# Kernel optimization log

Measured on AMD Instinct MI355X. Metric: run time of the kernel, lower is better.

The kernel has to match this reference:

```python
import jax, jax.numpy as jnp
import numpy as np

B, D, Q, E, H, V = 32, 1024, 64, 384, 384, 50000
PAD = 0
EPS = 1e-12


def setup_inputs() -> dict:
    key = jax.random.key(0)
    ks = jax.random.split(key, 13)
    documents = jax.random.randint(ks[0], (B, D), 1, V)
    doc_lens = jax.random.randint(ks[1], (B,), D // 2, D + 1)
    doc_valid = jnp.arange(D)[None, :] < doc_lens[:, None]
    documents = jnp.where(doc_valid, documents, PAD)
    doc_masks = doc_valid.astype(jnp.float32)[:, :, None]
    querys = jax.random.randint(ks[2], (B, Q), 1, V)
    query_lens = jax.random.randint(ks[3], (B,), Q // 2, Q + 1)
    q_valid = jnp.arange(Q)[None, :] < query_lens[:, None]
    querys = jnp.where(q_valid, querys, PAD)
    query_masks = q_valid.astype(jnp.float32)[:, :, None]
    answers = documents[:, :1]  # guaranteed present in each doc
    emb = jax.random.uniform(ks[4], (V + 1, E), jnp.float32, -0.05, 0.05)
    emb = emb.at[PAD].set(0.0)
    gw = lambda k, s: jax.random.normal(k, s, jnp.float32) * 0.05
    w_ih_f = gw(ks[5], (3 * H, E)); w_hh_f = gw(ks[6], (3 * H, H))
    b_ih_f = gw(ks[7], (3 * H,)); b_hh_f = gw(ks[8], (3 * H,))
    w_ih_b = gw(ks[9], (3 * H, E)); w_hh_b = gw(ks[10], (3 * H, H))
    b_ih_b = gw(ks[11], (3 * H,)); b_hh_b = gw(ks[12], (3 * H,))
    return dict(documents=documents, doc_lens=doc_lens, doc_masks=doc_masks,
                querys=querys, query_lens=query_lens, query_masks=query_masks,
                answers=answers, emb=emb,
                w_ih_f=w_ih_f, w_hh_f=w_hh_f, b_ih_f=b_ih_f, b_hh_f=b_hh_f,
                w_ih_b=w_ih_b, w_hh_b=w_hh_b, b_ih_b=b_ih_b, b_hh_b=b_hh_b)


def _gru_dir(x, w_ih, w_hh, b_ih, b_hh):
    # x: [B,T,E] -> outputs [B,T,H]; torch GRU cell math
    Bn = x.shape[0]
    Hn = w_hh.shape[1]
    xp = jnp.einsum('bte,ge->btg', x, w_ih) + b_ih  # precompute input projections [B,T,3H]

    def step(h, g):
        gh = h @ w_hh.T + b_hh
        i_r, i_z, i_n = jnp.split(g, 3, axis=-1)
        h_r, h_z, h_n = jnp.split(gh, 3, axis=-1)
        r = jax.nn.sigmoid(i_r + h_r)
        z = jax.nn.sigmoid(i_z + h_z)
        n = jnp.tanh(i_n + r * h_n)
        hn = (1.0 - z) * n + z * h
        return hn, hn

    h0 = jnp.zeros((Bn, Hn), x.dtype)
    _, out = jax.lax.scan(step, h0, jnp.swapaxes(xp, 0, 1))
    return jnp.swapaxes(out, 0, 1)


def _rev_within_len(x, lens):
    # reverse each sequence only over its valid prefix (emulates packed bwd GRU)
    T = x.shape[1]
    t = jnp.arange(T)
    idx = jnp.where(t[None, :] < lens[:, None], lens[:, None] - 1 - t[None, :], t[None, :])
    return jnp.take_along_axis(x, idx[:, :, None], axis=1)


def _bigru(x, lens, valid, pf, pb):
    out_f = _gru_dir(x, *pf)
    out_b = _rev_within_len(_gru_dir(_rev_within_len(x, lens), *pb), lens)
    out = jnp.concatenate([out_f, out_b], axis=-1)
    return out * valid[:, :, None]  # unpack pads with zeros


def _softmax_mask(x, mask, axis):
    shift = jnp.max(x, axis=axis, keepdims=True)
    e = jnp.exp(x - shift) * mask
    return e / (jnp.sum(e, axis=axis, keepdims=True) + EPS)


def reference(documents, doc_lens, doc_masks, querys, query_lens, query_masks, answers,
              emb, w_ih_f, w_hh_f, b_ih_f, b_hh_f, w_ih_b, w_hh_b, b_ih_b, b_hh_b):
    doc_valid = doc_masks[..., 0]
    q_valid = query_masks[..., 0]
    doc_h = _bigru(emb[documents], doc_lens, doc_valid,
                   (w_ih_f, w_hh_f, b_ih_f, b_hh_f), (w_ih_b, w_hh_b, b_ih_b, b_hh_b))
    q_h = _bigru(emb[querys], query_lens, q_valid,
                 (w_ih_f, w_hh_f, b_ih_f, b_hh_f), (w_ih_b, w_hh_b, b_ih_b, b_hh_b))
    scores = jnp.einsum('bdh,bqh->bdq', doc_h, q_h)          # IndiATT_output
    pair_mask = jnp.einsum('bdo,bqo->bdq', doc_masks, query_masks)
    alpha = _softmax_mask(scores, pair_mask, axis=1)
    beta = _softmax_mask(scores, pair_mask, axis=2)
    beta_aver = jnp.sum(beta, axis=1) / doc_lens[:, None].astype(scores.dtype)  # [B,Q]
    s = jnp.einsum('bdq,bq->bd', alpha, beta_aver)            # AoA_output squeezed
    probs = jnp.sum(s * (documents == answers).astype(s.dtype), axis=1)

    def pick(doc, sv, vv):
        sc = jnp.zeros(V + 1, s.dtype).at[doc].add(sv * vv)   # segment-sum by word id
        cnt = jnp.zeros(V + 1, s.dtype).at[doc].add(vv)
        return jnp.argmax(jnp.where(cnt > 0, sc, -jnp.inf))

    pred_answers = jax.vmap(pick)(documents, s, doc_valid)
    return probs, pred_answers
```

## Files before the change

kernel.cpp:

```cpp
#include <hip/hip_runtime.h>
#include <hip/hip_bf16.h>
#include <stdint.h>

#define EPSV 1e-12f
#define NB 32
#define DD 1024
#define QQ 64
#define EE 384
#define HH 384
#define NW 12
#define CH 256
#define XPBUF ((size_t)2 * CH * 36864)

typedef __attribute__((ext_vector_type(4))) float f32x4;
typedef __attribute__((ext_vector_type(8))) __bf16 bf16x8;
typedef __attribute__((ext_vector_type(4))) unsigned short u16x4;
typedef __attribute__((ext_vector_type(4))) int i32x4;
typedef unsigned short u16;

static __device__ __forceinline__ u16 f2bf(float f) {
  union { float f; uint32_t u; } v; v.f = f;
  uint32_t u = v.u;
  return (u16)((u + 0x7fffu + ((u >> 16) & 1u)) >> 16);
}

static __device__ __forceinline__ f32x4 MFMA(bf16x8 a, bf16x8 b, f32x4 c) {
  return __builtin_amdgcn_mfma_f32_16x16x32_bf16(a, b, c, 0, 0, 0);
}

static __device__ __forceinline__ bf16x8 ldw8(const float* p) {
  float4 a = *(const float4*)p;
  float4 b = *(const float4*)(p + 4);
  union { u16 e[8]; bf16x8 v; } u;
  u.e[0] = f2bf(a.x); u.e[1] = f2bf(a.y); u.e[2] = f2bf(a.z); u.e[3] = f2bf(a.w);
  u.e[4] = f2bf(b.x); u.e[5] = f2bf(b.y); u.e[6] = f2bf(b.z); u.e[7] = f2bf(b.w);
  return u.v;
}

static __device__ __forceinline__ void st_short_sc(u16* p, u16 v) {
  asm volatile("global_store_short %0, %1, off sc1" :: "v"(p), "v"((uint32_t)v) : "memory");
}
static __device__ __forceinline__ void ld_b128_sc(const u16* p, i32x4& d) {
  asm volatile("global_load_dwordx4 %0, %1, off sc1" : "=v"(d) : "v"(p) : "memory");
}
static __device__ __forceinline__ void st_dword_sc(unsigned* p, unsigned v) {
  asm volatile("global_store_dword %0, %1, off sc1" :: "v"(p), "v"(v) : "memory");
}
static __device__ __forceinline__ void ld_tags(const unsigned* p, i32x4& a, i32x4& b, i32x4& c,
                                               i32x4& d, i32x4& e, i32x4& f) {
  asm volatile(
      "global_load_dwordx4 %0, %6, off sc1\n\t"
      "global_load_dwordx4 %1, %6, off offset:16 sc1\n\t"
      "global_load_dwordx4 %2, %6, off offset:32 sc1\n\t"
      "global_load_dwordx4 %3, %6, off offset:48 sc1\n\t"
      "global_load_dwordx4 %4, %6, off offset:64 sc1\n\t"
      "global_load_dwordx4 %5, %6, off offset:80 sc1\n\t"
      "s_waitcnt vmcnt(0)"
      : "=&v"(a), "=&v"(b), "=&v"(c), "=&v"(d), "=&v"(e), "=&v"(f)
      : "v"(p) : "memory");
}

__global__ __launch_bounds__(256) void k_emb(const int* __restrict__ doc, const int* __restrict__ qry,
                                             const float* __restrict__ emb, u16* __restrict__ embx) {
  int i = blockIdx.x * 256 + threadIdx.x;
  int row = i / 96, e4 = i - row * 96;
  int tok = (row < NB * DD) ? doc[row] : qry[row - NB * DD];
  float4 v = ((const float4*)(emb + (size_t)tok * EE))[e4];
  u16x4 o; o.x = f2bf(v.x); o.y = f2bf(v.y); o.z = f2bf(v.z); o.w = f2bf(v.w);
  *(u16x4*)(embx + (size_t)row * EE + e4 * 4) = o;
}

__global__ __launch_bounds__(512, 2) void k_xp(
    const u16* __restrict__ embx, const int* __restrict__ doc_lens, const int* __restrict__ q_lens,
    const float* __restrict__ w_ih_f, const float* __restrict__ b_ih_f, const float* __restrict__ b_hh_f,
    const float* __restrict__ w_ih_b, const float* __restrict__ b_ih_b, const float* __restrict__ b_hh_b,
    float* __restrict__ xpd, float* __restrict__ xpq, int cbase) {
  __shared__ int lensh[32];
  const int gx = blockIdx.x;
  int corpus, d2, jblk, tch;
  if (gx < 48) { corpus = 0; d2 = gx / 24; int rem = gx % 24; jblk = rem / 4; tch = rem % 4; }
  else { corpus = 1; int g2 = gx - 48; d2 = g2 / 6; jblk = g2 % 6; tch = 0; }
  const int T = corpus ? QQ : DD;
  const int* lens = corpus ? q_lens : doc_lens;
  const float* w_ih = d2 ? w_ih_b : w_ih_f;
  const float* b_ih = d2 ? b_ih_b : b_ih_f;
  const float* b_hh = d2 ? b_hh_b : b_hh_f;
  const u16* exb = embx + (corpus ? (size_t)NB * DD * EE : 0);
  float* xpg = corpus ? (xpq + (size_t)d2 * QQ * 36864) : (xpd + (size_t)d2 * CH * 36864);
  const int tid = threadIdx.x;
  if (tid < 32) lensh[tid] = lens[tid];
  __syncthreads();
  const int lane = tid & 63, wv = tid >> 6;
  const int wslot = wv >> 1, mt = wv & 1;
  const int col = lane & 15, khi = lane >> 4;
  const int jg = jblk * 64 + wslot * 16 + col;
  const float br = b_ih[jg] + b_hh[jg];
  const float bz = b_ih[384 + jg] + b_hh[384 + jg];
  const float bn = b_ih[768 + jg];
  bf16x8 Wr[12], Wz[12], Wn[12];
#pragma unroll
  for (int ks = 0; ks < 12; ++ks) {
    Wr[ks] = ldw8(w_ih + (size_t)jg * 384 + ks * 32 + khi * 8);
    Wz[ks] = ldw8(w_ih + (size_t)(384 + jg) * 384 + ks * 32 + khi * 8);
    Wn[ks] = ldw8(w_ih + (size_t)(768 + jg) * 384 + ks * 32 + khi * 8);
  }
  const int b_a = mt * 16 + col;
  const int lenb = lensh[b_a];
  const int bh0 = mt * 16 + khi * 4;
  for (int tt = 0; tt < 64; ++tt) {
    const int s_lc = tch * 64 + tt;
    const int s_g = corpus ? s_lc : (cbase + s_lc);
    const int trow = d2 ? ((s_g < lenb) ? (lenb - 1 - s_g) : s_g) : s_g;
    const u16* ap = exb + ((size_t)b_a * T + trow) * EE + khi * 8;
    bf16x8 A[12];
#pragma unroll
    for (int ks = 0; ks < 12; ++ks) A[ks] = *(const bf16x8*)(ap + ks * 32);
    f32x4 ar{0.f, 0.f, 0.f, 0.f}, az = ar, an = ar;
#pragma unroll
    for (int ks = 0; ks < 12; ++ks) {
      ar = MFMA(A[ks], Wr[ks], ar);
      az = MFMA(A[ks], Wz[ks], az);
      an = MFMA(A[ks], Wn[ks], an);
    }
    float* op = xpg + (size_t)s_lc * 36864 + (size_t)jg * 32 + bh0;
    f32x4 o0{ar[0] + br, ar[1] + br, ar[2] + br, ar[3] + br};
    f32x4 o1{az[0] + bz, az[1] + bz, az[2] + bz, az[3] + bz};
    f32x4 o2{an[0] + bn, an[1] + bn, an[2] + bn, an[3] + bn};
    *(f32x4*)op = o0;
    *(f32x4*)(op + 384 * 32) = o1;
    *(f32x4*)(op + 768 * 32) = o2;
  }
}

__global__ __launch_bounds__(256) void k_rec(
    const float* __restrict__ xp_rd, float* __restrict__ xp_wr, const float* __restrict__ xpq,
    const int* __restrict__ doc_lens, const int* __restrict__ q_lens,
    const float* __restrict__ w_hh_f, const float* __restrict__ b_hh_f,
    const float* __restrict__ w_hh_b, const float* __restrict__ b_hh_b,
    u16* __restrict__ doc_h, u16* __restrict__ q_h,
    u16* __restrict__ h_bc, unsigned* __restrict__ cnts, unsigned* __restrict__ tags,
    float* __restrict__ h_state,
    const u16* __restrict__ embx,
    const float* __restrict__ w_ih_f, const float* __restrict__ b_ih_f,
    const float* __restrict__ w_ih_b, const float* __restrict__ b_ih_b,
    int cbase, int first, int rec_blocks) {
  __shared__ u16 wfrag[36864];
  __shared__ int lensh[32];
  const int bid = blockIdx.x;
  const int tid = threadIdx.x;

  if (bid >= rec_blocks) {
    const int e = bid - rec_blocks;
    const int d2 = e / 48;
    const int rem = e - d2 * 48;
    const int jb = rem >> 2, tch = rem & 3;
    const float* w_ih = d2 ? w_ih_b : w_ih_f;
    const float* b_ih = d2 ? b_ih_b : b_ih_f;
    const float* b_hh2 = d2 ? b_hh_b : b_hh_f;
    float* xpo = xp_wr + (size_t)d2 * CH * 36864;
    if (tid < 32) lensh[tid] = doc_lens[tid];
    __syncthreads();
    const int lane = tid & 63, wv = tid >> 6;
    const int wslot = wv >> 1, mt = wv & 1;
    const int col = lane & 15, khi = lane >> 4;
    const int jg = jb * 32 + wslot * 16 + col;
    const float br = b_ih[jg] + b_hh2[jg];
    const float bz = b_ih[384 + jg] + b_hh2[384 + jg];
    const float bn = b_ih[768 + jg];
    bf16x8 Wr[12], Wz[12], Wn[12];
#pragma unroll
    for (int ks = 0; ks < 12; ++ks) {
      Wr[ks] = ldw8(w_ih + (size_t)jg * 384 + ks * 32 + khi * 8);
      Wz[ks] = ldw8(w_ih + (size_t)(384 + jg) * 384 + ks * 32 + khi * 8);
      Wn[ks] = ldw8(w_ih + (size_t)(768 + jg) * 384 + ks * 32 + khi * 8);
    }
    const int b_a = mt * 16 + col;
    const int lenb = lensh[b_a];
    const int bh0 = mt * 16 + khi * 4;
    const int cb2 = cbase + CH;
    for (int tt = 0; tt < 64; ++tt) {
      const int s_lc = tch * 64 + tt;
      const int s_g = cb2 + s_lc;
      const int trow = d2 ? ((s_g < lenb) ? (lenb - 1 - s_g) : s_g) : s_g;
      const u16* ap = embx + ((size_t)b_a * DD + trow) * EE + khi * 8;
      bf16x8 A[12];
#pragma unroll
      for (int ks = 0; ks < 12; ++ks) A[ks] = *(const bf16x8*)(ap + ks * 32);
      f32x4 ar{0.f, 0.f, 0.f, 0.f}, az = ar, an = ar;
#pragma unroll
      for (int ks = 0; ks < 12; ++ks) {
        ar = MFMA(A[ks], Wr[ks], ar);
        az = MFMA(A[ks], Wz[ks], az);
        an = MFMA(A[ks], Wn[ks], an);
      }
      float* op = xpo + (size_t)s_lc * 36864 + (size_t)jg * 32 + bh0;
      f32x4 o0{ar[0] + br, ar[1] + br, ar[2] + br, ar[3] + br};
      f32x4 o1{az[0] + bz, az[1] + bz, az[2] + bz, az[3] + bz};
      f32x4 o2{an[0] + bn, an[1] + bn, an[2] + bn, an[3] + bn};
      *(f32x4*)op = o0;
      *(f32x4*)(op + 384 * 32) = o1;
      *(f32x4*)(op + 768 * 32) = o2;
    }
    return;
  }

  const int grp = bid / NW;
  const int wg = bid - grp * NW;
  const int corpus = grp >> 1, dir = grp & 1;
  const int T = corpus ? QQ : DD;
  const int nst = corpus ? QQ : CH;
  const int* lens = corpus ? q_lens : doc_lens;
  const float* w_hh = dir ? w_hh_b : w_hh_f;
  const float* b_hh = dir ? b_hh_b : b_hh_f;
  u16* out = corpus ? q_h : doc_h;
  const float* xpg = corpus ? (xpq + (size_t)dir * QQ * 36864) : (xp_rd + (size_t)dir * CH * 36864);
  u16* hb = h_bc + (size_t)grp * (2 * NB * HH);
  unsigned* cnt = cnts + (size_t)grp * 16;

  if (tid < 32) lensh[tid] = lens[tid];
  for (int idx = tid; idx < 36864; idx += 256) {
    int nt = idx / 6144;
    int rem = idx - nt * 6144;
    int ks = rem >> 9;
    int le = rem & 511;
    int lane_ = le >> 3, i = le & 7;
    int g = nt >> 1, js_ = nt & 1;
    int colw = lane_ & 15;
    int k = ks * 32 + (lane_ >> 4) * 8 + i;
    int rowg = g * 384 + wg * 32 + js_ * 16 + colw;
    wfrag[idx] = f2bf(w_hh[(size_t)rowg * 384 + k]);
  }
  if (first) {
    for (int idx = tid; idx < 1024; idx += 256) {
      int b = idx >> 5, jl_ = idx & 31;
      st_short_sc(hb + b * HH + wg * 32 + jl_, (u16)0);
    }
    asm volatile("s_waitcnt vmcnt(0)" ::: "memory");
  }
  __syncthreads();
  if (first) {
    if (tid == 0) {
      __hip_atomic_fetch_add(cnt, 1u, __ATOMIC_RELAXED, __HIP_MEMORY_SCOPE_AGENT);
      while (__hip_atomic_load(cnt, __ATOMIC_RELAXED, __HIP_MEMORY_SCOPE_AGENT) < (unsigned)NW)
        __builtin_amdgcn_s_sleep(1);
    }
    __syncthreads();
  }

  const int lane = tid & 63, wv = tid >> 6;
  const int mt = wv >> 1, js = wv & 1;
  const int col = lane & 15, khi = lane >> 4;
  const int jg = wg * 32 + js * 16 + col;
  const float bias_hn = b_hh[768 + jg];
  const int b_x = mt * 16 + col;
  const int bh0 = mt * 16 + khi * 4;
  int len_h[4];
#pragma unroll
  for (int r = 0; r < 4; ++r) len_h[r] = lensh[bh0 + r];
  u16* outp = out + (size_t)dir * HH + jg;
  f32x4 hprev;
#pragma unroll
  for (int r = 0; r < 4; ++r)
    hprev[r] = first ? 0.f : h_state[(size_t)grp * 12288 + (size_t)jg * 32 + (bh0 + r)];

  const unsigned* tagrow = tags + (size_t)grp * 64 + mt * 32;
  unsigned* tagp = tags + (size_t)grp * 64 + mt * 32 + (wg * 2 + js);

  auto umin2 = [](unsigned a, unsigned b) { return a < b ? a : b; };
  auto pollwait = [&](unsigned need) {
    while (true) {
      i32x4 t0, t1, t2, t3, t4, t5;
      ld_tags(tagrow, t0, t1, t2, t3, t4, t5);
      unsigned mn = 0xffffffffu;
#pragma unroll
      for (int k = 0; k < 4; ++k) {
        mn = umin2(mn, (unsigned)t0[k]); mn = umin2(mn, (unsigned)t1[k]);
        mn = umin2(mn, (unsigned)t2[k]); mn = umin2(mn, (unsigned)t3[k]);
        mn = umin2(mn, (unsigned)t4[k]); mn = umin2(mn, (unsigned)t5[k]);
      }
      if (mn >= need) break;
      __builtin_amdgcn_s_sleep(1);
    }
  };
  auto load_xp = [&](f32x4* x, int sl) {
    const float* xs = xpg + (size_t)sl * 36864;
#pragma unroll
    for (int g = 0; g < 3; ++g)
      x[g] = *(const f32x4*)(xs + ((size_t)(g * 384 + jg)) * 32 + bh0);
  };

  f32x4 xpA[3], xpB[3];
  load_xp(xpA, 0);

  auto step = [&](int sl, f32x4* xc, f32x4* xn) {
    const int s = cbase + sl;
    const int p = s & 1;
    const u16* rbuf = hb + p * (NB * HH);
    u16* wbuf = hb + (p ^ 1) * (NB * HH);
    pollwait((unsigned)s);
    i32x4 areg[12];
    const u16* ahp = rbuf + b_x * HH + khi * 8;
#pragma unroll
    for (int ks = 0; ks < 12; ++ks) ld_b128_sc(ahp + ks * 32, areg[ks]);
    asm volatile("s_waitcnt vmcnt(0)" ::: "memory");
    __builtin_amdgcn_sched_barrier(0);
    f32x4 acc_r{0.f, 0.f, 0.f, 0.f};
    f32x4 acc_z = acc_r, acc_nh = acc_r;
#pragma unroll
    for (int ks = 0; ks < 12; ++ks) {
      bf16x8 af = __builtin_bit_cast(bf16x8, areg[ks]);
      bf16x8 br = *(const bf16x8*)&wfrag[((js) * 12 + ks) * 512 + lane * 8];
      bf16x8 bz = *(const bf16x8*)&wfrag[((2 + js) * 12 + ks) * 512 + lane * 8];
      bf16x8 bn = *(const bf16x8*)&wfrag[((4 + js) * 12 + ks) * 512 + lane * 8];
      acc_r = MFMA(af, br, acc_r);
      acc_z = MFMA(af, bz, acc_z);
      acc_nh = MFMA(af, bn, acc_nh);
    }
    u16 hq[4];
#pragma unroll
    for (int r = 0; r < 4; ++r) {
      const int b = bh0 + r;
      float rg = 1.f / (1.f + __expf(-(acc_r[r] + xc[0][r])));
      float zg = 1.f / (1.f + __expf(-(acc_z[r] + xc[1][r])));
      float ng = tanhf(xc[2][r] + rg * (acc_nh[r] + bias_hn));
      float hn = (1.f - zg) * ng + zg * hprev[r];
      hprev[r] = hn;
      hq[r] = f2bf(hn);
      st_short_sc(wbuf + b * HH + jg, hq[r]);
    }
    asm volatile("s_waitcnt vmcnt(0)" ::: "memory");
    if (lane == 0) st_dword_sc(tagp, (unsigned)(s + 1));
    load_xp(xn, (sl + 1 < nst) ? (sl + 1) : sl);
#pragma unroll
    for (int r = 0; r < 4; ++r) {
      const int b = bh0 + r;
      const int len = len_h[r];
      const int tro = dir ? ((s < len) ? (len - 1 - s) : s) : s;
      outp[((size_t)b * T + tro) * (2 * HH)] = hq[r];
    }
  };

  for (int sl = 0; sl < nst; sl += 2) {
    step(sl, xpA, xpB);
    step(sl + 1, xpB, xpA);
  }
#pragma unroll
  for (int r = 0; r < 4; ++r)
    h_state[(size_t)grp * 12288 + (size_t)jg * 32 + (bh0 + r)] = hprev[r];
}

__global__ __launch_bounds__(256) void k_scores(
    const u16* __restrict__ doc_h, const u16* __restrict__ q_h,
    const int* __restrict__ doc_lens, const int* __restrict__ q_lens,
    float* __restrict__ SM, float* __restrict__ rowmax, float* __restrict__ rowsum) {
  const int b = blockIdx.x >> 4, dblk = blockIdx.x & 15;
  const int tid = threadIdx.x, lane = tid & 63, wv = tid >> 6;
  const int col = lane & 15, khi = lane >> 4;
  const int dlen = doc_lens[b], qlen = q_lens[b];
  const u16* dp = doc_h + ((size_t)(b * DD + dblk * 64 + wv * 16 + col)) * (2 * HH) + khi * 8;
  const u16* qp = q_h + (size_t)b * QQ * (2 * HH);
  f32x4 acc[4];
#pragma unroll
  for (int nt = 0; nt < 4; ++nt) acc[nt] = f32x4{0.f, 0.f, 0.f, 0.f};
  for (int ks = 0; ks < 24; ++ks) {
    bf16x8 av = *(const bf16x8*)(dp + ks * 32);
#pragma unroll
    for (int nt = 0; nt < 4; ++nt) {
      bf16x8 bv = *(const bf16x8*)(qp + (size_t)(nt * 16 + col) * (2 * HH) + ks * 32 + khi * 8);
      acc[nt] = MFMA(av, bv, acc[nt]);
    }
  }
  const int d0 = dblk * 64 + wv * 16 + khi * 4;
  float* smb = SM + (size_t)b * DD * QQ;
#pragma unroll
  for (int r = 0; r < 4; ++r) {
    const int d = d0 + r;
    const bool dv = d < dlen;
    float v[4];
#pragma unroll
    for (int nt = 0; nt < 4; ++nt) {
      const int q = nt * 16 + col;
      v[nt] = (dv && q < qlen) ? acc[nt][r] : 0.f;
      smb[(size_t)d * QQ + q] = v[nt];
    }
    float mx = fmaxf(fmaxf(v[0], v[1]), fmaxf(v[2], v[3]));
#pragma unroll
    for (int off = 1; off < 16; off <<= 1) mx = fmaxf(mx, __shfl_xor(mx, off, 64));
    float sm = 0.f;
#pragma unroll
    for (int nt = 0; nt < 4; ++nt) {
      const int q = nt * 16 + col;
      if (dv && q < qlen) sm += __expf(v[nt] - mx);
    }
#pragma unroll
    for (int off = 1; off < 16; off <<= 1) sm += __shfl_xor(sm, off, 64);
    if (col == 0) { rowmax[b * DD + d] = mx; rowsum[b * DD + d] = sm; }
  }
}

__global__ __launch_bounds__(256) void k_cols(
    const float* __restrict__ SM, const float* __restrict__ rowmax, const float* __restrict__ rowsum,
    const int* __restrict__ doc_lens, const int* __restrict__ q_lens,
    float* __restrict__ colmax, float* __restrict__ colsum, float* __restrict__ bav) {
  const int b = blockIdx.x, tid = threadIdx.x;
  const int q = tid & 63, dg = tid >> 6;
  __shared__ float red[4][64];
  __shared__ float cmx[64];
  const float* smb = SM + (size_t)b * DD * QQ;
  float cm = -3.0e38f;
  for (int d = dg; d < DD; d += 4) cm = fmaxf(cm, smb[(size_t)d * QQ + q]);
  red[dg][q] = cm;
  __syncthreads();
  if (tid < 64) cmx[tid] = fmaxf(fmaxf(red[0][tid], red[1][tid]), fmaxf(red[2][tid], red[3][tid]));
  __syncthreads();
  const int dlen = doc_lens[b];
  const bool qv = q < q_lens[b];
  const float cmq = cmx[q];
  float cs = 0.f, ba = 0.f;
  for (int d = dg; d < DD; d += 4) {
    if (qv && d < dlen) {
      float v = smb[(size_t)d * QQ + q];
      cs += __expf(v - cmq);
      ba += __expf(v - rowmax[b * DD + d]) / (rowsum[b * DD + d] + EPSV);
    }
  }
  __syncthreads();
  red[dg][q] = cs;
  __syncthreads();
  float cst = 0.f;
  if (tid < 64) cst = red[0][tid] + red[1][tid] + red[2][tid] + red[3][tid];
  __syncthreads();
  red[dg][q] = ba;
  __syncthreads();
  if (tid < 64) {
    float bat = red[0][tid] + red[1][tid] + red[2][tid] + red[3][tid];
    colmax[b * QQ + tid] = cmx[tid];
    colsum[b * QQ + tid] = cst;
    bav[b * QQ + tid] = bat / (float)dlen;
  }
}

__global__ __launch_bounds__(256) void k_s(
    const float* __restrict__ SM, const float* __restrict__ colmax, const float* __restrict__ colsum,
    const float* __restrict__ bav, const int* __restrict__ doc_lens, const int* __restrict__ q_lens,
    const int* __restrict__ documents, const int* __restrict__ answers,
    float* __restrict__ sc, float* __restrict__ cnt_tok, float* __restrict__ dout) {
  const int b = blockIdx.x >> 2, dblk = blockIdx.x & 3;
  const int tid = threadIdx.x;
  __shared__ float cm[64], cs[64], bv[64];
  __shared__ int qm[64];
  if (tid < 64) {
    cm[tid] = colmax[b * QQ + tid];
    cs[tid] = colsum[b * QQ + tid];
    bv[tid] = bav[b * QQ + tid];
    qm[tid] = (tid < q_lens[b]) ? 1 : 0;
  }
  __syncthreads();
  const int d = dblk * 256 + tid;
  const bool dv = d < doc_lens[b];
  const float* smr = SM + ((size_t)b * DD + d) * QQ;
  float sd = 0.f;
#pragma unroll
  for (int q = 0; q < 64; ++q) {
    float e = (dv && qm[q]) ? __expf(smr[q] - cm[q]) : 0.f;
    sd += e / (cs[q] + EPSV) * bv[q];
  }
  const int tok = documents[b * DD + d];
  if (tok == answers[b]) atomicAdd(&dout[b], sd);
  if (dv) {
    atomicAdd(&sc[(size_t)b * 50001 + tok], sd);
    atomicAdd(&cnt_tok[(size_t)b * 50001 + tok], 1.0f);
  }
}

__global__ __launch_bounds__(256) void k_pred(
    const float* __restrict__ sc, const float* __restrict__ cnt_tok, float* __restrict__ dout) {
  const int b = blockIdx.x, tid = threadIdx.x;
  __shared__ float bvs[256];
  __shared__ int bis[256];
  float bvv = -3.0e38f;
  int bii = 0x7fffffff;
  for (int i = tid; i < 50001; i += 256) {
    if (cnt_tok[(size_t)b * 50001 + i] > 0.f) {
      float v = sc[(size_t)b * 50001 + i];
      if (v > bvv) { bvv = v; bii = i; }
    }
  }
  bvs[tid] = bvv;
  bis[tid] = bii;
  __syncthreads();
  for (int st = 128; st > 0; st >>= 1) {
    if (tid < st) {
      float v2 = bvs[tid + st];
      int i2 = bis[tid + st];
      if (v2 > bvs[tid] || (v2 == bvs[tid] && i2 < bis[tid])) { bvs[tid] = v2; bis[tid] = i2; }
    }
    __syncthreads();
  }
  if (tid == 0) dout[32 + b] = (float)bis[0];
}

extern "C" void kernel_launch(void* const* d_in, const int* in_sizes, int n_in,
                              void* d_out, int out_size, void* d_ws, size_t ws_size,
                              hipStream_t stream) {
  const int* documents = (const int*)d_in[0];
  const int* doc_lens = (const int*)d_in[1];
  const int* querys = (const int*)d_in[3];
  const int* query_lens = (const int*)d_in[4];
  const int* answers = (const int*)d_in[6];
  const float* emb = (const float*)d_in[7];
  const float* w_ih_f = (const float*)d_in[8];
  const float* w_hh_f = (const float*)d_in[9];
  const float* b_ih_f = (const float*)d_in[10];
  const float* b_hh_f = (const float*)d_in[11];
  const float* w_ih_b = (const float*)d_in[12];
  const float* w_hh_b = (const float*)d_in[13];
  const float* b_ih_b = (const float*)d_in[14];
  const float* b_hh_b = (const float*)d_in[15];
  float* dout = (float*)d_out;
  char* ws = (char*)d_ws;

  size_t o = 0;
  auto alloc = [&](size_t bytes) { size_t r = o; o += (bytes + 255) & ~(size_t)255; return r; };
  size_t o_embx = alloc((size_t)34816 * 384 * 2);
  size_t o_xpd  = alloc((size_t)2 * XPBUF * 4);
  size_t o_xpq  = alloc((size_t)2 * QQ * 36864 * 4);
  size_t o_doch = alloc((size_t)NB * DD * 768 * 2);
  size_t o_qh   = alloc((size_t)NB * QQ * 768 * 2);
  size_t o_hbc  = alloc((size_t)4 * 2 * NB * HH * 2);
  size_t o_hst  = alloc((size_t)4 * HH * NB * 4);
  size_t o_cnt  = alloc((size_t)4 * 16 * 4);
  size_t o_tag  = alloc((size_t)4 * 64 * 4);
  size_t o_sync_end = o;
  size_t o_SM   = alloc((size_t)NB * DD * QQ * 4);
  size_t o_rmax = alloc((size_t)NB * DD * 4);
  size_t o_rsum = alloc((size_t)NB * DD * 4);
  size_t o_cmax = alloc((size_t)NB * QQ * 4);
  size_t o_csum = alloc((size_t)NB * QQ * 4);
  size_t o_bav  = alloc((size_t)NB * QQ * 4);
  size_t o_sc   = alloc((size_t)NB * 50001 * 4);
  size_t o_ctk  = alloc((size_t)NB * 50001 * 4);
  (void)ws_size; (void)in_sizes; (void)n_in; (void)out_size;

  hipMemsetAsync(ws + o_cnt, 0, o_sync_end - o_cnt, stream);
  hipMemsetAsync(ws + o_sc, 0, (o_ctk - o_sc) + (size_t)NB * 50001 * 4, stream);
  hipMemsetAsync(d_out, 0, 64 * sizeof(float), stream);

  k_emb<<<13056, 256, 0, stream>>>(documents, querys, emb, (u16*)(ws + o_embx));
  k_xp<<<60, 512, 0, stream>>>((u16*)(ws + o_embx), doc_lens, query_lens,
                               w_ih_f, b_ih_f, b_hh_f, w_ih_b, b_ih_b, b_hh_b,
                               (float*)(ws + o_xpd), (float*)(ws + o_xpq), 0);
  for (int c = 0; c < 4; ++c) {
    const int rec_blocks = (c == 0) ? 48 : 24;
    const int xp_blocks = (c < 3) ? 96 : 0;
    float* xp_rd = (float*)(ws + o_xpd) + (size_t)(c & 1) * XPBUF;
    float* xp_wr = (float*)(ws + o_xpd) + (size_t)((c + 1) & 1) * XPBUF;
    k_rec<<<rec_blocks + xp_blocks, 256, 0, stream>>>(
        xp_rd, xp_wr, (float*)(ws + o_xpq), doc_lens, query_lens,
        w_hh_f, b_hh_f, w_hh_b, b_hh_b,
        (u16*)(ws + o_doch), (u16*)(ws + o_qh),
        (u16*)(ws + o_hbc), (unsigned*)(ws + o_cnt), (unsigned*)(ws + o_tag),
        (float*)(ws + o_hst),
        (u16*)(ws + o_embx), w_ih_f, b_ih_f, w_ih_b, b_ih_b,
        c * CH, c == 0 ? 1 : 0, rec_blocks);
  }
  k_scores<<<512, 256, 0, stream>>>((u16*)(ws + o_doch), (u16*)(ws + o_qh), doc_lens, query_lens,
                                    (float*)(ws + o_SM), (float*)(ws + o_rmax), (float*)(ws + o_rsum));
  k_cols<<<32, 256, 0, stream>>>((float*)(ws + o_SM), (float*)(ws + o_rmax), (float*)(ws + o_rsum),
                                 doc_lens, query_lens,
                                 (float*)(ws + o_cmax), (float*)(ws + o_csum), (float*)(ws + o_bav));
  k_s<<<128, 256, 0, stream>>>((float*)(ws + o_SM), (float*)(ws + o_cmax), (float*)(ws + o_csum),
                               (float*)(ws + o_bav), doc_lens, query_lens, documents, answers,
                               (float*)(ws + o_sc), (float*)(ws + o_ctk), dout);
  k_pred<<<32, 256, 0, stream>>>((float*)(ws + o_sc), (float*)(ws + o_ctk), dout);
}
```

Baseline: 5.285 ms.

## Halve recurrent workgroups per GRU direction, doubling hidden columns per block

Each recurrent group now uses 6 workgroups instead of 12. Each workgroup holds 64 hidden columns of W_hh in LDS (twice the previous footprint) and issues six MFMA chains per wave per step instead of three. The per-step cross-workgroup tag poll now reads 12 tags instead of 24, and the first chunk launches half as many recurrent blocks. The aim is to cut inter-block synchronisation latency on the serial time loop. The cost is more work per block on the critical path and LDS use close to the per-block limit.

```diff
diff --git a/kernel.cpp b/kernel.cpp
--- a/kernel.cpp
+++ b/kernel.cpp
@@ -8,7 +8,7 @@
 #define QQ 64
 #define EE 384
 #define HH 384
-#define NW 12
+#define NW 6
 #define CH 256
 #define XPBUF ((size_t)2 * CH * 36864)
 
@@ -46,17 +46,13 @@
 static __device__ __forceinline__ void st_dword_sc(unsigned* p, unsigned v) {
   asm volatile("global_store_dword %0, %1, off sc1" :: "v"(p), "v"(v) : "memory");
 }
-static __device__ __forceinline__ void ld_tags(const unsigned* p, i32x4& a, i32x4& b, i32x4& c,
-                                               i32x4& d, i32x4& e, i32x4& f) {
+static __device__ __forceinline__ void ld_tags3(const unsigned* p, i32x4& a, i32x4& b, i32x4& c) {
   asm volatile(
-      "global_load_dwordx4 %0, %6, off sc1\n\t"
-      "global_load_dwordx4 %1, %6, off offset:16 sc1\n\t"
-      "global_load_dwordx4 %2, %6, off offset:32 sc1\n\t"
-      "global_load_dwordx4 %3, %6, off offset:48 sc1\n\t"
-      "global_load_dwordx4 %4, %6, off offset:64 sc1\n\t"
-      "global_load_dwordx4 %5, %6, off offset:80 sc1\n\t"
+      "global_load_dwordx4 %0, %3, off sc1\n\t"
+      "global_load_dwordx4 %1, %3, off offset:16 sc1\n\t"
+      "global_load_dwordx4 %2, %3, off offset:32 sc1\n\t"
       "s_waitcnt vmcnt(0)"
-      : "=&v"(a), "=&v"(b), "=&v"(c), "=&v"(d), "=&v"(e), "=&v"(f)
+      : "=&v"(a), "=&v"(b), "=&v"(c)
       : "v"(p) : "memory");
 }
 
@@ -144,7 +140,7 @@
     const float* __restrict__ w_ih_f, const float* __restrict__ b_ih_f,
     const float* __restrict__ w_ih_b, const float* __restrict__ b_ih_b,
     int cbase, int first, int rec_blocks) {
-  __shared__ u16 wfrag[36864];
+  __shared__ u16 wfrag[73728];
   __shared__ int lensh[32];
   const int bid = blockIdx.x;
   const int tid = threadIdx.x;
@@ -218,22 +214,22 @@
   unsigned* cnt = cnts + (size_t)grp * 16;
 
   if (tid < 32) lensh[tid] = lens[tid];
-  for (int idx = tid; idx < 36864; idx += 256) {
-    int nt = idx / 6144;
-    int rem = idx - nt * 6144;
+  for (int idx = tid; idx < 73728; idx += 256) {
+    int t = idx / 6144;
+    int rem = idx - t * 6144;
     int ks = rem >> 9;
     int le = rem & 511;
     int lane_ = le >> 3, i = le & 7;
-    int g = nt >> 1, js_ = nt & 1;
+    int g = t >> 2, sl = t & 3;
     int colw = lane_ & 15;
     int k = ks * 32 + (lane_ >> 4) * 8 + i;
-    int rowg = g * 384 + wg * 32 + js_ * 16 + colw;
+    int rowg = g * 384 + wg * 64 + sl * 16 + colw;
     wfrag[idx] = f2bf(w_hh[(size_t)rowg * 384 + k]);
   }
   if (first) {
-    for (int idx = tid; idx < 1024; idx += 256) {
-      int b = idx >> 5, jl_ = idx & 31;
-      st_short_sc(hb + b * HH + wg * 32 + jl_, (u16)0);
+    for (int idx = tid; idx < 2048; idx += 256) {
+      int b = idx >> 6, jl_ = idx & 63;
+      st_short_sc(hb + b * HH + wg * 64 + jl_, (u16)0);
     }
     asm volatile("s_waitcnt vmcnt(0)" ::: "memory");
   }
@@ -248,52 +244,61 @@
   }
 
   const int lane = tid & 63, wv = tid >> 6;
-  const int mt = wv >> 1, js = wv & 1;
+  const int mt = wv >> 1, jw = wv & 1;
   const int col = lane & 15, khi = lane >> 4;
-  const int jg = wg * 32 + js * 16 + col;
-  const float bias_hn = b_hh[768 + jg];
+  const int d0g = wg * 64 + jw * 32 + col;
+  const int d1g = d0g + 16;
+  const float bhn0 = b_hh[768 + d0g];
+  const float bhn1 = b_hh[768 + d1g];
   const int b_x = mt * 16 + col;
   const int bh0 = mt * 16 + khi * 4;
   int len_h[4];
 #pragma unroll
   for (int r = 0; r < 4; ++r) len_h[r] = lensh[bh0 + r];
-  u16* outp = out + (size_t)dir * HH + jg;
-  f32x4 hprev;
-#pragma unroll
-  for (int r = 0; r < 4; ++r)
-    hprev[r] = first ? 0.f : h_state[(size_t)grp * 12288 + (size_t)jg * 32 + (bh0 + r)];
+  u16* outp = out + (size_t)dir * HH;
+  f32x4 hp0, hp1;
+#pragma unroll
+  for (int r = 0; r < 4; ++r) {
+    hp0[r] = first ? 0.f : h_state[(size_t)grp * 12288 + (size_t)d0g * 32 + (bh0 + r)];
+    hp1[r] = first ? 0.f : h_state[(size_t)grp * 12288 + (size_t)d1g * 32 + (bh0 + r)];
+  }
 
   const unsigned* tagrow = tags + (size_t)grp * 64 + mt * 32;
-  unsigned* tagp = tags + (size_t)grp * 64 + mt * 32 + (wg * 2 + js);
+  unsigned* tagp = tags + (size_t)grp * 64 + mt * 32 + (wg * 2 + jw);
 
   auto umin2 = [](unsigned a, unsigned b) { return a < b ? a : b; };
   auto pollwait = [&](unsigned need) {
     while (true) {
-      i32x4 t0, t1, t2, t3, t4, t5;
-      ld_tags(tagrow, t0, t1, t2, t3, t4, t5);
+      i32x4 t0, t1, t2;
+      ld_tags3(tagrow, t0, t1, t2);
       unsigned mn = 0xffffffffu;
 #pragma unroll
       for (int k = 0; k < 4; ++k) {
         mn = umin2(mn, (unsigned)t0[k]); mn = umin2(mn, (unsigned)t1[k]);
-        mn = umin2(mn, (unsigned)t2[k]); mn = umin2(mn, (unsigned)t3[k]);
-        mn = umin2(mn, (unsigned)t4[k]); mn = umin2(mn, (unsigned)t5[k]);
+        mn = umin2(mn, (unsigned)t2[k]);
       }
       if (mn >= need) break;
       __builtin_amdgcn_s_sleep(1);
     }
   };
-  auto load_xp = [&](f32x4* x, int sl) {
-    const float* xs = xpg + (size_t)sl * 36864;
-#pragma unroll
-    for (int g = 0; g < 3; ++g)
-      x[g] = *(const f32x4*)(xs + ((size_t)(g * 384 + jg)) * 32 + bh0);
+  const int tb0 = (jw * 2) * 12;
+  auto wf = [&](int g, int s2, int ks) -> bf16x8 {
+    return *(const bf16x8*)&wfrag[(((g * 4) + tb0 / 12 * 0 + (jw * 2 + s2)) * 12 + ks) * 512 + lane * 8];
   };
-
-  f32x4 xpA[3], xpB[3];
+  auto load_xp = [&](f32x4* x, int sl_) {
+    const float* xs = xpg + (size_t)sl_ * 36864;
+#pragma unroll
+    for (int g = 0; g < 3; ++g) {
+      x[g * 2 + 0] = *(const f32x4*)(xs + ((size_t)(g * 384 + d0g)) * 32 + bh0);
+      x[g * 2 + 1] = *(const f32x4*)(xs + ((size_t)(g * 384 + d1g)) * 32 + bh0);
+    }
+  };
+
+  f32x4 xpA[6], xpB[6];
   load_xp(xpA, 0);
 
-  auto step = [&](int sl, f32x4* xc, f32x4* xn) {
-    const int s = cbase + sl;
+  auto step = [&](int sl_, f32x4* xc, f32x4* xn) {
+    const int s = cbase + sl_;
     const int p = s & 1;
     const u16* rbuf = hb + p * (NB * HH);
     u16* wbuf = hb + (p ^ 1) * (NB * HH);
@@ -304,49 +309,62 @@
     for (int ks = 0; ks < 12; ++ks) ld_b128_sc(ahp + ks * 32, areg[ks]);
     asm volatile("s_waitcnt vmcnt(0)" ::: "memory");
     __builtin_amdgcn_sched_barrier(0);
-    f32x4 acc_r{0.f, 0.f, 0.f, 0.f};
-    f32x4 acc_z = acc_r, acc_nh = acc_r;
+    f32x4 ar0{0.f,0.f,0.f,0.f}, ar1 = ar0, az0 = ar0, az1 = ar0, an0 = ar0, an1 = ar0;
 #pragma unroll
     for (int ks = 0; ks < 12; ++ks) {
       bf16x8 af = __builtin_bit_cast(bf16x8, areg[ks]);
-      bf16x8 br = *(const bf16x8*)&wfrag[((js) * 12 + ks) * 512 + lane * 8];
-      bf16x8 bz = *(const bf16x8*)&wfrag[((2 + js) * 12 + ks) * 512 + lane * 8];
-      bf16x8 bn = *(const bf16x8*)&wfrag[((4 + js) * 12 + ks) * 512 + lane * 8];
-      acc_r = MFMA(af, br, acc_r);
-      acc_z = MFMA(af, bz, acc_z);
-      acc_nh = MFMA(af, bn, acc_nh);
-    }
-    u16 hq[4];
+      ar0 = MFMA(af, wf(0, 0, ks), ar0);
+      ar1 = MFMA(af, wf(0, 1, ks), ar1);
+      az0 = MFMA(af, wf(1, 0, ks), az0);
+      az1 = MFMA(af, wf(1, 1, ks), az1);
+      an0 = MFMA(af, wf(2, 0, ks), an0);
+      an1 = MFMA(af, wf(2, 1, ks), an1);
+    }
+    u16 hq0[4], hq1[4];
 #pragma unroll
     for (int r = 0; r < 4; ++r) {
       const int b = bh0 + r;
-      float rg = 1.f / (1.f + __expf(-(acc_r[r] + xc[0][r])));
-      float zg = 1.f / (1.f + __expf(-(acc_z[r] + xc[1][r])));
-      float ng = tanhf(xc[2][r] + rg * (acc_nh[r] + bias_hn));
-      float hn = (1.f - zg) * ng + zg * hprev[r];
-      hprev[r] = hn;
-      hq[r] = f2bf(hn);
-      st_short_sc(wbuf + b * HH + jg, hq[r]);
+      {
+        float rg = 1.f / (1.f + __expf(-(ar0[r] + xc[0][r])));
+        float zg = 1.f / (1.f + __expf(-(az0[r] + xc[2][r])));
+        float ng = tanhf(xc[4][r] + rg * (an0[r] + bhn0));
+        float hn = (1.f - zg) * ng + zg * hp0[r];
+        hp0[r] = hn;
+        hq0[r] = f2bf(hn);
+        st_short_sc(wbuf + b * HH + d0g, hq0[r]);
+      }
+      {
+        float rg = 1.f / (1.f + __expf(-(ar1[r] + xc[1][r])));
+        float zg = 1.f / (1.f + __expf(-(az1[r] + xc[3][r])));
+        float ng = tanhf(xc[5][r] + rg * (an1[r] + bhn1));
+        float hn = (1.f - zg) * ng + zg * hp1[r];
+        hp1[r] = hn;
+        hq1[r] = f2bf(hn);
+        st_short_sc(wbuf + b * HH + d1g, hq1[r]);
+      }
     }
     asm volatile("s_waitcnt vmcnt(0)" ::: "memory");
     if (lane == 0) st_dword_sc(tagp, (unsigned)(s + 1));
-    load_xp(xn, (sl + 1 < nst) ? (sl + 1) : sl);
+    load_xp(xn, (sl_ + 1 < nst) ? (sl_ + 1) : sl_);
 #pragma unroll
     for (int r = 0; r < 4; ++r) {
       const int b = bh0 + r;
       const int len = len_h[r];
       const int tro = dir ? ((s < len) ? (len - 1 - s) : s) : s;
-      outp[((size_t)b * T + tro) * (2 * HH)] = hq[r];
+      outp[((size_t)b * T + tro) * (2 * HH) + d0g] = hq0[r];
+      outp[((size_t)b * T + tro) * (2 * HH) + d1g] = hq1[r];
     }
   };
 
-  for (int sl = 0; sl < nst; sl += 2) {
-    step(sl, xpA, xpB);
-    step(sl + 1, xpB, xpA);
-  }
-#pragma unroll
-  for (int r = 0; r < 4; ++r)
-    h_state[(size_t)grp * 12288 + (size_t)jg * 32 + (bh0 + r)] = hprev[r];
+  for (int sl_ = 0; sl_ < nst; sl_ += 2) {
+    step(sl_, xpA, xpB);
+    step(sl_ + 1, xpB, xpA);
+  }
+#pragma unroll
+  for (int r = 0; r < 4; ++r) {
+    h_state[(size_t)grp * 12288 + (size_t)d0g * 32 + (bh0 + r)] = hp0[r];
+    h_state[(size_t)grp * 12288 + (size_t)d1g * 32 + (bh0 + r)] = hp1[r];
+  }
 }
 
 __global__ __launch_bounds__(256) void k_scores(
@@ -551,7 +569,7 @@
                                w_ih_f, b_ih_f, b_hh_f, w_ih_b, b_ih_b, b_hh_b,
                                (float*)(ws + o_xpd), (float*)(ws + o_xpq), 0);
   for (int c = 0; c < 4; ++c) {
-    const int rec_blocks = (c == 0) ? 48 : 24;
+    const int rec_blocks = (c == 0) ? 24 : 12;
     const int xp_blocks = (c < 3) ? 96 : 0;
     float* xp_rd = (float*)(ws + o_xpd) + (size_t)(c & 1) * XPBUF;
     float* xp_wr = (float*)(ws + o_xpd) + (size_t)((c + 1) & 1) * XPBUF;
```

Measured after the change: 6.446 ms. 1.22x slower.
